# Performance work log

Hardware: AMD Instinct MI355X
Metric: run time of the kernel (lower is better)

Reference implementation:

```python
import jax, jax.numpy as jnp
import numpy as np

B, C, TX, TY = 32, 384, 512, 2048
NL, K = 2, 3
EPS = 1e-5


def _ln(x, g, b):
    # channel-wise LayerNorm over dim 1 of [B, C, T]
    m = jnp.mean(x, axis=1, keepdims=True)
    v = jnp.mean((x - m) ** 2, axis=1, keepdims=True)
    return (x - m) * jax.lax.rsqrt(v + EPS) * g[None, :, None] + b[None, :, None]


def _conv(x, w, b):
    # x: [B, C, T], w: [O, I, K] -> 'SAME' padding == kernel_size // 2 for odd K
    y = jax.lax.conv_general_dilated(x, w, (1,), 'SAME',
                                     dimension_numbers=('NCH', 'OIH', 'NCH'))
    return y + b[None, :, None]


def _variance_predictor(x, mask, lng, lnb, cw, cb, ow, ob):
    # NL x (LayerNorm -> Conv1d -> SiLU -> [dropout=identity in eval]) * mask
    for i in range(NL):
        h = _conv(_ln(x, lng[i], lnb[i]), cw[i], cb[i])
        x = jax.nn.silu(h) * mask
    return _conv(x, ow, ob) * mask  # [B, 1, T]


def setup_inputs() -> dict:
    key = jax.random.key(0)
    it = iter(jax.random.split(key, 16))
    s = 0.02
    d = {}
    d['x'] = jax.random.normal(next(it), (B, C, TX), jnp.float32)
    d['x_mask'] = jnp.ones((B, 1, TX), jnp.float32)
    d['y_mask'] = jnp.ones((B, 1, TY), jnp.float32)
    d['pitch'] = jax.random.normal(next(it), (B, C, TY), jnp.float32)
    d['energy'] = jax.random.normal(next(it), (B, C, TY), jnp.float32)
    d['path'] = jax.random.uniform(next(it), (B, TX, TY), jnp.float32)
    for p in ('dur', 'pit', 'ene'):
        d[p + '_lng'] = jnp.ones((NL, C), jnp.float32)
        d[p + '_lnb'] = jnp.zeros((NL, C), jnp.float32)
        d[p + '_cw'] = jax.random.normal(next(it), (NL, C, C, K), jnp.float32) * s
        d[p + '_cb'] = jnp.zeros((NL, C), jnp.float32)
        d[p + '_ow'] = jax.random.normal(next(it), (1, C, 1), jnp.float32) * s
        d[p + '_ob'] = jnp.zeros((1,), jnp.float32)
    return d


def reference(x, x_mask, y_mask, pitch, energy, path,
              dur_lng, dur_lnb, dur_cw, dur_cb, dur_ow, dur_ob,
              pit_lng, pit_lnb, pit_cw, pit_cb, pit_ow, pit_ob,
              ene_lng, ene_lnb, ene_cw, ene_cb, ene_ow, ene_ob):
    dur_pred = _variance_predictor(x, x_mask, dur_lng, dur_lnb, dur_cw, dur_cb, dur_ow, dur_ob)
    # LengthRegulator: bmm against duration path matrix [B, TX, TY]
    xe = jnp.einsum('bct,bty->bcy', x, path)  # [B, C, TY]
    pitch_pred = _variance_predictor(xe, y_mask, pit_lng, pit_lnb, pit_cw, pit_cb, pit_ow, pit_ob)
    energy_pred = _variance_predictor(xe, y_mask, ene_lng, ene_lnb, ene_cw, ene_cb, ene_ow, ene_ob)
    out = xe + pitch + energy
    return (out, dur_pred, pitch_pred, energy_pred)
```

## Files before the change

### kernel.cpp

```cpp
#include <hip/hip_runtime.h>

#define B_ 32
#define C_ 384
#define TX_ 512
#define TY_ 2048
#define KW_ 3
#define EPS_ 1e-5f
#define LAY_ ((size_t)(36 * 1536 * 8))

typedef __attribute__((ext_vector_type(8))) short short8;
typedef __attribute__((ext_vector_type(4))) float f32x4;

#define MFMA(a, b, c) __builtin_amdgcn_mfma_f32_16x16x32_bf16(a, b, c, 0, 0, 0)

#define WAITV0() do { asm volatile("s_waitcnt vmcnt(0)"); \
                      __builtin_amdgcn_sched_barrier(0); } while (0)
#define WAITL()  do { asm volatile("s_waitcnt lgkmcnt(0)"); \
                      __builtin_amdgcn_sched_barrier(0); } while (0)

typedef unsigned int u32;
__device__ __forceinline__ void gl_lds16(const void* g, void* l) {
    __builtin_amdgcn_global_load_lds(
        (const __attribute__((address_space(1))) u32*)g,
        (__attribute__((address_space(3))) u32*)l, 16, 0, 0);
}

__device__ inline unsigned short f2bf(float f) {
    union { float f; unsigned int u; } v; v.f = f;
    unsigned int r = v.u + 0x7fffu + ((v.u >> 16) & 1u);
    return (unsigned short)(r >> 16);
}
__device__ inline float bf2f(unsigned short s) {
    union { float f; unsigned int u; } v; v.u = ((unsigned int)s) << 16;
    return v.f;
}

template<bool INBF>
__device__ inline float ldx(const void* p, size_t i) {
    if constexpr (INBF) return bf2f(((const unsigned short*)p)[i]);
    else return ((const float*)p)[i];
}

__global__ __launch_bounds__(256) void pack_w2(const float* cw0, const float* cw1,
                                               const float* cw2, const float* g0,
                                               const float* g1, const float* g2,
                                               unsigned short* wp) {
    int idx = blockIdx.x * 256 + threadIdx.x;
    const int NG = 6 * 36 * 384 * 4;
    if (idx >= NG) return;
    int lg = idx & 3;
    int o = (idx >> 2) % 384;
    int c = ((idx >> 2) / 384) % 36;
    int lay = (idx >> 2) / (384 * 36);
    int k = c / 12, ib = c % 12;
    int pr = lay >> 1, l = lay & 1;
    const float* cw = ((pr == 0) ? cw0 : (pr == 1) ? cw1 : cw2) + (size_t)l * C_ * C_ * KW_;
    const float* g  = ((pr == 0) ? g0  : (pr == 1) ? g1  : g2)  + (size_t)l * C_;
    const int i0 = ib * 32 + lg * 8;
    short8 v;
    #pragma unroll
    for (int e = 0; e < 8; e++)
        v[e] = (short)f2bf(cw[((size_t)o * C_ + i0 + e) * KW_ + k] * g[i0 + e]);
    *(short8*)&wp[(size_t)idx * 8] = v;
}

__global__ __launch_bounds__(256) void bias_fold(
    const float* cw0, const float* cw1, const float* cw2,
    const float* be0, const float* be1, const float* be2,
    const float* cb0, const float* cb1, const float* cb2,
    float* biasT, float* bc0, float* bc2) {
    int idx = blockIdx.x * 256 + threadIdx.x;
    if (idx >= 6 * 384) return;
    int o = idx % 384, lay = idx / 384;
    int pr = lay >> 1, l = lay & 1;
    const float* cw = ((pr == 0) ? cw0 : (pr == 1) ? cw1 : cw2)
                      + (size_t)l * C_ * C_ * KW_ + (size_t)o * C_ * KW_;
    const float* be = ((pr == 0) ? be0 : (pr == 1) ? be1 : be2) + (size_t)l * C_;
    const float* cb = ((pr == 0) ? cb0 : (pr == 1) ? cb1 : cb2) + (size_t)l * C_;
    float s0 = 0.f, s1 = 0.f, s2 = 0.f;
    for (int i = 0; i < C_; i++) {
        const float b = be[i];
        s0 += cw[i * 3 + 0] * b; s1 += cw[i * 3 + 1] * b; s2 += cw[i * 3 + 2] * b;
    }
    biasT[idx] = cb[o] + s0 + s1 + s2;
    bc0[idx] = s0; bc2[idx] = s2;
}

__global__ __launch_bounds__(256) void pack_x2(const float* x, unsigned short* xp) {
    int idx = blockIdx.x * 256 + threadIdx.x;
    const int NG = B_ * 16 * 384 * 4;
    if (idx >= NG) return;
    int lg = idx & 3;
    int c = (idx >> 2) % 384;
    int q = ((idx >> 2) / 384) % 16;
    int b = (idx >> 2) / (384 * 16);
    const float* src = x + ((size_t)b * C_ + c) * TX_ + q * 32 + lg * 8;
    short8 v;
    #pragma unroll
    for (int e = 0; e < 8; e++) v[e] = (short)f2bf(src[e]);
    *(short8*)&xp[(size_t)idx * 8] = v;
}

__global__ __launch_bounds__(256) void ln_stats_f32(const float* x, float2* st, int T) {
    __shared__ float r1[4][64], r2[4][64];
    int b = blockIdx.y, t0 = blockIdx.x * 64;
    int tl = threadIdx.x & 63, g = threadIdx.x >> 6;
    int t = t0 + tl;
    const float* p = x + (size_t)b * C_ * T + t;
    float s = 0.f, ss = 0.f;
    for (int c = g; c < C_; c += 4) { float v = p[(size_t)c * T]; s += v; ss += v * v; }
    r1[g][tl] = s; r2[g][tl] = ss;
    __syncthreads();
    if (threadIdx.x < 64) {
        float s1 = r1[0][tl] + r1[1][tl] + r1[2][tl] + r1[3][tl];
        float s2 = r2[0][tl] + r2[1][tl] + r2[2][tl] + r2[3][tl];
        float m = s1 * (1.f / C_);
        float var = s2 * (1.f / C_) - m * m;
        st[(size_t)b * T + t0 + tl] = make_float2(m, rsqrtf(var + EPS_));
    }
}

template<bool INBF>
__global__ __launch_bounds__(512, 4) void fused_vp(
    const void* __restrict__ Xin, const float2* __restrict__ stin,
    const unsigned short* __restrict__ W2lay,
    const float* __restrict__ bT,
    const float* __restrict__ c0v, const float* __restrict__ c2v,
    const float* __restrict__ mask,
    float* __restrict__ pred, const float* __restrict__ ow,
    const float* __restrict__ obias, int T)
{
    __shared__ __align__(16) unsigned short xs[68 * 384];
    __shared__ __align__(16) unsigned short wlds[8][1536];
    float*  red = (float*) &xs[66 * 384];
    float2* st2 = (float2*)&xs[67 * 384];

    const int tid = threadIdx.x;
    const int b = blockIdx.y;
    const int t0 = blockIdx.x * 64;
    const int lane = tid & 63;
    const int wave = tid >> 6;
    const int lr = lane & 15, lg = lane >> 4;
    const int wm = wave * 48;

    const unsigned short* gbw = W2lay + (size_t)((wm + lr) * 4 + lg) * 8;
    const unsigned short* gbw2 = gbw + LAY_;
    auto STAGE = [&](const unsigned short* base, int c) {
        #pragma unroll
        for (int fm = 0; fm < 3; fm++)
            gl_lds16(base + (size_t)c * 12288 + fm * 512, &wlds[wave][fm * 512]);
    };
    STAGE(gbw, 0);

    {
        const int tt = 2 + lane;
        const int t = t0 + lane;
        const float2 mr = stin[(size_t)b * T + t];
        for (int cg = wave; cg < 48; cg += 8) {
            const size_t base = ((size_t)b * C_ + cg * 8) * T + t;
            short8 v8;
            #pragma unroll
            for (int j = 0; j < 8; j++)
                v8[j] = (short)f2bf((ldx<INBF>(Xin, base + (size_t)j * T) - mr.x) * mr.y);
            const int ph = (cg & ~7) | ((cg ^ tt) & 7);
            *(short8*)&xs[tt * 384 + ph * 8] = v8;
        }
        if (tid < 192) {
            const int q = tid / 48;
            const int tt2 = (q < 2) ? q : 64 + q;
            const int cg = tid % 48;
            const int t2 = t0 - 2 + tt2;
            short8 v8;
            if (t2 >= 0 && t2 < T) {
                const float2 mr2 = stin[(size_t)b * T + t2];
                const size_t base = ((size_t)b * C_ + cg * 8) * T + t2;
                #pragma unroll
                for (int j = 0; j < 8; j++)
                    v8[j] = (short)f2bf((ldx<INBF>(Xin, base + (size_t)j * T) - mr2.x) * mr2.y);
            } else {
                #pragma unroll
                for (int j = 0; j < 8; j++) v8[j] = 0;
            }
            const int ph = (cg & ~7) | ((cg ^ tt2) & 7);
            *(short8*)&xs[tt2 * 384 + ph * 8] = v8;
        }
    }
    __syncthreads();

    f32x4 acc[3][5];
    const f32x4 zero = {0.f, 0.f, 0.f, 0.f};
    #pragma unroll
    for (int fm = 0; fm < 3; fm++)
        #pragma unroll
        for (int fn = 0; fn < 5; fn++) acc[fm][fn] = zero;

    for (int c = 0; c < 36; ++c) {
        WAITV0();
        short8 af[3], bf[5];
        #pragma unroll
        for (int fm = 0; fm < 3; fm++)
            af[fm] = *(const short8*)&wlds[wave][fm * 512 + lane * 8];
        const int k = c / 12, ib = c - k * 12;
        const int cgi = ib * 4 + lg;
        #pragma unroll
        for (int fn = 0; fn < 4; fn++) {
            const int row = 1 + fn * 16 + lr + k;
            const int ph = (cgi & ~7) | ((cgi ^ row) & 7);
            bf[fn] = *(const short8*)&xs[row * 384 + ph * 8];
        }
        {
            const int row = (lr == 1) ? (65 + k) : k;
            const int ph = (cgi & ~7) | ((cgi ^ row) & 7);
            bf[4] = *(const short8*)&xs[row * 384 + ph * 8];
        }
        WAITL();
        if (c < 35) STAGE(gbw, c + 1); else STAGE(gbw2, 0);
        __builtin_amdgcn_sched_barrier(0);
        __builtin_amdgcn_s_setprio(1);
        #pragma unroll
        for (int fm = 0; fm < 3; fm++)
            #pragma unroll
            for (int fn = 0; fn < 5; fn++)
                acc[fm][fn] = MFMA(af[fm], bf[fn], acc[fm][fn]);
        __builtin_amdgcn_s_setprio(0);
    }

    __syncthreads();
    if (tid < 132) red[tid] = 0.f;
    __syncthreads();

    #pragma unroll
    for (int fn = 0; fn < 4; fn++) {
        const int tt_h = 1 + fn * 16 + lr;
        const int t = t0 + fn * 16 + lr;
        const float mk = mask[(size_t)b * T + t];
        float s1 = 0.f, s2 = 0.f;
        #pragma unroll
        for (int fm = 0; fm < 3; fm++) {
            const int o0 = wm + fm * 16 + lg * 4;
            #pragma unroll
            for (int j = 0; j < 4; j++) {
                float h = acc[fm][fn][j] + bT[o0 + j];
                if (t == 0) h -= c0v[o0 + j];
                if (t == T - 1) h -= c2v[o0 + j];
                const float y = h * (1.f / (1.f + __expf(-h))) * mk;
                acc[fm][fn][j] = y;
                s1 += y; s2 += y * y;
            }
        }
        atomicAdd(&red[tt_h * 2], s1);
        atomicAdd(&red[tt_h * 2 + 1], s2);
    }
    {
        const int tt_h = (lr == 1) ? 65 : 0;
        const int t = t0 - 1 + tt_h;
        const bool inr = (lr < 2) && (t >= 0) && (t < T);
        const float mk = inr ? mask[(size_t)b * T + t] : 0.f;
        float s1 = 0.f, s2 = 0.f;
        #pragma unroll
        for (int fm = 0; fm < 3; fm++) {
            const int o0 = wm + fm * 16 + lg * 4;
            #pragma unroll
            for (int j = 0; j < 4; j++) {
                const float h = acc[fm][4][j] + bT[o0 + j];
                const float y = inr ? (h * (1.f / (1.f + __expf(-h))) * mk) : 0.f;
                acc[fm][4][j] = y;
                s1 += y; s2 += y * y;
            }
        }
        if (inr) {
            atomicAdd(&red[tt_h * 2], s1);
            atomicAdd(&red[tt_h * 2 + 1], s2);
        }
    }
    __syncthreads();

    if (tid < 66) {
        const float s1 = red[tid * 2], s2 = red[tid * 2 + 1];
        const float m = s1 * (1.f / C_);
        const float var = s2 * (1.f / C_) - m * m;
        st2[tid] = make_float2(m, rsqrtf(var + EPS_));
    }
    __syncthreads();

    #pragma unroll
    for (int fn = 0; fn < 4; fn++) {
        const int tt_h = 1 + fn * 16 + lr;
        const float2 mr = st2[tt_h];
        #pragma unroll
        for (int fm = 0; fm < 3; fm++) {
            ushort4 pk;
            #pragma unroll
            for (int j = 0; j < 4; j++)
                ((unsigned short*)&pk)[j] = f2bf((acc[fm][fn][j] - mr.x) * mr.y);
            const int cg = ((wm + fm * 16) >> 3) + (lg >> 1);
            const int ph = (cg & ~7) | ((cg ^ tt_h) & 7);
            *(ushort4*)&xs[tt_h * 384 + ph * 8 + (lg & 1) * 4] = pk;
        }
    }
    if (lr < 2) {
        const int tt_h = (lr == 1) ? 65 : 0;
        const float2 mr = st2[tt_h];
        #pragma unroll
        for (int fm = 0; fm < 3; fm++) {
            ushort4 pk;
            #pragma unroll
            for (int j = 0; j < 4; j++)
                ((unsigned short*)&pk)[j] = f2bf((acc[fm][4][j] - mr.x) * mr.y);
            const int cg = ((wm + fm * 16) >> 3) + (lg >> 1);
            const int ph = (cg & ~7) | ((cg ^ tt_h) & 7);
            *(ushort4*)&xs[tt_h * 384 + ph * 8 + (lg & 1) * 4] = pk;
        }
    }
    __syncthreads();

    f32x4 acc2[3][4];
    #pragma unroll
    for (int fm = 0; fm < 3; fm++)
        #pragma unroll
        for (int fn = 0; fn < 4; fn++) acc2[fm][fn] = zero;

    for (int c = 0; c < 36; ++c) {
        WAITV0();
        short8 af[3], bf[4];
        #pragma unroll
        for (int fm = 0; fm < 3; fm++)
            af[fm] = *(const short8*)&wlds[wave][fm * 512 + lane * 8];
        const int k = c / 12, ib = c - k * 12;
        const int cgi = ib * 4 + lg;
        #pragma unroll
        for (int fn = 0; fn < 4; fn++) {
            const int row = fn * 16 + lr + k;
            const int ph = (cgi & ~7) | ((cgi ^ row) & 7);
            bf[fn] = *(const short8*)&xs[row * 384 + ph * 8];
        }
        WAITL();
        if (c < 35) STAGE(gbw2, c + 1);
        __builtin_amdgcn_sched_barrier(0);
        __builtin_amdgcn_s_setprio(1);
        #pragma unroll
        for (int fm = 0; fm < 3; fm++)
            #pragma unroll
            for (int fn = 0; fn < 4; fn++)
                acc2[fm][fn] = MFMA(af[fm], bf[fn], acc2[fm][fn]);
        __builtin_amdgcn_s_setprio(0);
    }

    __syncthreads();
    if (tid < 64) red[tid] = 0.f;
    __syncthreads();
    #pragma unroll
    for (int fn = 0; fn < 4; fn++) {
        const int tl = fn * 16 + lr;
        const int t = t0 + tl;
        const float mk = mask[(size_t)b * T + t];
        float s1 = 0.f;
        #pragma unroll
        for (int fm = 0; fm < 3; fm++) {
            const int o0 = wm + fm * 16 + lg * 4;
            #pragma unroll
            for (int j = 0; j < 4; j++) {
                float h = acc2[fm][fn][j] + bT[384 + o0 + j];
                if (t == 0) h -= c0v[384 + o0 + j];
                if (t == T - 1) h -= c2v[384 + o0 + j];
                const float y = h * (1.f / (1.f + __expf(-h))) * mk;
                s1 += y * ow[o0 + j];
            }
        }
        atomicAdd(&red[tl], s1);
    }
    __syncthreads();
    if (tid < 64) {
        const int t = t0 + tid;
        pred[(size_t)b * T + t] = (red[tid] + obias[0]) * mask[(size_t)b * T + t];
    }
}

__global__ __launch_bounds__(512, 4) void bmm_ln(
    const unsigned short* __restrict__ x2, const float* __restrict__ path,
    const float* __restrict__ pitch, const float* __restrict__ energy,
    float* __restrict__ out, unsigned short* __restrict__ xebf,
    float2* __restrict__ stout, int fused)
{
    __shared__ __align__(16) unsigned short ps[32 * 512];
    __shared__ __align__(16) unsigned short wlds[8][1536];
    const int tid = threadIdx.x;
    const int bid = blockIdx.x;
    const int work = (bid & 7) * 256 + (bid >> 3);
    const int b = work >> 6;
    const int y0 = (work & 63) << 5;
    const int lane = tid & 63;
    const int wave = tid >> 6;
    const int lr = lane & 15, lg = lane >> 4;
    const int wm = wave * 48;

    const unsigned short* gbx = x2 + ((size_t)b * 16 * 1536 + (size_t)((wm + lr) * 4 + lg)) * 8;
    auto STAGE = [&](int u) {
        #pragma unroll
        for (int fm = 0; fm < 3; fm++)
            gl_lds16(gbx + (size_t)u * 12288 + fm * 512, &wlds[wave][fm * 512]);
    };
    STAGE(0);

    {
        const int yy = lane & 31;
        const int half = lane >> 5;
        const int gbase = (wave * 2 + half) * 4;
        const float* pb = path + (size_t)b * TX_ * TY_ + y0 + yy;
        float vv[4][8];
        #pragma unroll
        for (int i = 0; i < 4; i++) {
            const int cg = gbase + i;
            #pragma unroll
            for (int j = 0; j < 8; j++) vv[i][j] = pb[(size_t)(cg * 8 + j) * TY_];
        }
        #pragma unroll
        for (int i = 0; i < 4; i++) {
            const int cg = gbase + i;
            short8 v8;
            #pragma unroll
            for (int j = 0; j < 8; j++) v8[j] = (short)f2bf(vv[i][j]);
            const int ph = (cg & ~7) | ((cg ^ yy) & 7);
            *(short8*)&ps[yy * 512 + ph * 8] = v8;
        }
    }
    __syncthreads();

    f32x4 acc[3][2];
    const f32x4 zero = {0.f, 0.f, 0.f, 0.f};
    #pragma unroll
    for (int fm = 0; fm < 3; fm++) { acc[fm][0] = zero; acc[fm][1] = zero; }

    for (int u = 0; u < 16; ++u) {
        WAITV0();
        short8 af[3], bf[2];
        #pragma unroll
        for (int fm = 0; fm < 3; fm++)
            af[fm] = *(const short8*)&wlds[wave][fm * 512 + lane * 8];
        const int cgi = u * 4 + lg;
        #pragma unroll
        for (int fn = 0; fn < 2; fn++) {
            const int row = fn * 16 + lr;
            const int ph = (cgi & ~7) | ((cgi ^ row) & 7);
            bf[fn] = *(const short8*)&ps[row * 512 + ph * 8];
        }
        WAITL();
        if (u < 15) STAGE(u + 1);
        __builtin_amdgcn_sched_barrier(0);
        __builtin_amdgcn_s_setprio(1);
        #pragma unroll
        for (int fm = 0; fm < 3; fm++) {
            acc[fm][0] = MFMA(af[fm], bf[0], acc[fm][0]);
            acc[fm][1] = MFMA(af[fm], bf[1], acc[fm][1]);
        }
        __builtin_amdgcn_s_setprio(0);
    }

    __syncthreads();
    float* red = (float*)ps;
    if (tid < 64) red[tid] = 0.f;
    __syncthreads();

    #pragma unroll
    for (int fn = 0; fn < 2; fn++) {
        const int yl = fn * 16 + lr;
        const int y = y0 + yl;
        float s1 = 0.f, s2 = 0.f;
        #pragma unroll
        for (int fm = 0; fm < 3; fm++) {
            #pragma unroll
            for (int j = 0; j < 4; j++) {
                const int c = wm + fm * 16 + lg * 4 + j;
                const size_t gi = ((size_t)b * C_ + c) * TY_ + y;
                const float v = acc[fm][fn][j];
                if (fused) {
                    out[gi] = v + pitch[gi] + energy[gi];
                    xebf[gi] = f2bf(v);
                } else {
                    out[gi] = v;
                }
                s1 += v; s2 += v * v;
            }
        }
        atomicAdd(&red[yl * 2], s1);
        atomicAdd(&red[yl * 2 + 1], s2);
    }
    __syncthreads();
    if (tid < 32) {
        const int y = y0 + tid;
        const float s1 = red[tid * 2], s2 = red[tid * 2 + 1];
        const float m = s1 * (1.f / C_);
        const float var = s2 * (1.f / C_) - m * m;
        stout[(size_t)b * TY_ + y] = make_float2(m, rsqrtf(var + EPS_));
    }
}

__global__ __launch_bounds__(256) void add3(float4* o, const float4* p, const float4* e, int n4) {
    for (int i = blockIdx.x * 256 + threadIdx.x; i < n4; i += gridDim.x * 256) {
        float4 a = o[i], x1 = p[i], x2 = e[i];
        a.x += x1.x + x2.x; a.y += x1.y + x2.y;
        a.z += x1.z + x2.z; a.w += x1.w + x2.w;
        o[i] = a;
    }
}

extern "C" void kernel_launch(void* const* d_in, const int* in_sizes, int n_in,
                              void* d_out, int out_size, void* d_ws, size_t ws_size,
                              hipStream_t stream)
{
    const float* x      = (const float*)d_in[0];
    const float* x_mask = (const float*)d_in[1];
    const float* y_mask = (const float*)d_in[2];
    const float* pitch  = (const float*)d_in[3];
    const float* energy = (const float*)d_in[4];
    const float* path   = (const float*)d_in[5];
    const float* prm[3][6];
    for (int p = 0; p < 3; p++)
        for (int q = 0; q < 6; q++)
            prm[p][q] = (const float*)d_in[6 + p * 6 + q];

    float* out         = (float*)d_out;
    float* dur_pred    = out + (size_t)B_ * C_ * TY_;
    float* pitch_pred  = dur_pred + B_ * TX_;
    float* energy_pred = pitch_pred + B_ * TY_;

    const size_t BCTY = (size_t)B_ * C_ * TY_;
    char* w = (char*)d_ws;
    auto alloc = [&](size_t bytes) { char* r = w; w += (bytes + 255) & ~(size_t)255; return r; };

    unsigned short* W2   = (unsigned short*)alloc(6 * LAY_ * 2);
    float* biasT         = (float*)alloc(6 * 384 * 4);
    float* bc0           = (float*)alloc(6 * 384 * 4);
    float* bc2           = (float*)alloc(6 * 384 * 4);
    float2* stA          = (float2*)alloc((size_t)B_ * TY_ * 8);
    unsigned short* x2p  = (unsigned short*)alloc((size_t)B_ * 196608 * 2);
    size_t base_end = (size_t)(w - (char*)d_ws);
    unsigned short* xebf = (unsigned short*)alloc(BCTY * 2);
    size_t xe_end = (size_t)(w - (char*)d_ws);

    const bool haveXe = (xe_end <= ws_size);
    if (base_end > ws_size) return;

    pack_w2<<<dim3((6 * 36 * 384 * 4 + 255) / 256), 256, 0, stream>>>(
        prm[0][2], prm[1][2], prm[2][2], prm[0][0], prm[1][0], prm[2][0], W2);
    bias_fold<<<dim3(9), 256, 0, stream>>>(
        prm[0][2], prm[1][2], prm[2][2], prm[0][1], prm[1][1], prm[2][1],
        prm[0][3], prm[1][3], prm[2][3], biasT, bc0, bc2);
    pack_x2<<<dim3((B_ * 16 * 384 * 4 + 255) / 256), 256, 0, stream>>>(x, x2p);
    ln_stats_f32<<<dim3(TX_ / 64, B_), 256, 0, stream>>>(x, stA, TX_);

    fused_vp<false><<<dim3(TX_ / 64, B_), 512, 0, stream>>>(
        x, stA, W2, biasT, bc0, bc2, x_mask,
        dur_pred, prm[0][4], prm[0][5], TX_);

    bmm_ln<<<dim3(2048, 1, 1), 512, 0, stream>>>(
        x2p, path, pitch, energy, out, haveXe ? xebf : nullptr, stA, haveXe ? 1 : 0);

    if (haveXe) {
        fused_vp<true><<<dim3(TY_ / 64, B_), 512, 0, stream>>>(
            xebf, stA, W2 + 2 * LAY_, biasT + 2 * 384, bc0 + 2 * 384, bc2 + 2 * 384,
            y_mask, pitch_pred, prm[1][4], prm[1][5], TY_);
        fused_vp<true><<<dim3(TY_ / 64, B_), 512, 0, stream>>>(
            xebf, stA, W2 + 4 * LAY_, biasT + 4 * 384, bc0 + 4 * 384, bc2 + 4 * 384,
            y_mask, energy_pred, prm[2][4], prm[2][5], TY_);
    } else {
        fused_vp<false><<<dim3(TY_ / 64, B_), 512, 0, stream>>>(
            out, stA, W2 + 2 * LAY_, biasT + 2 * 384, bc0 + 2 * 384, bc2 + 2 * 384,
            y_mask, pitch_pred, prm[1][4], prm[1][5], TY_);
        fused_vp<false><<<dim3(TY_ / 64, B_), 512, 0, stream>>>(
            out, stA, W2 + 4 * LAY_, biasT + 4 * 384, bc0 + 4 * 384, bc2 + 4 * 384,
            y_mask, energy_pred, prm[2][4], prm[2][5], TY_);
        add3<<<dim3(2048), 256, 0, stream>>>((float4*)out, (const float4*)pitch,
                                             (const float4*)energy, B_ * C_ * TY_ / 4);
    }
}
```

Measured before the change: 644.3 us.

## Double the fused predictor time tile and double-buffer weight staging

The fused variance-predictor kernel now covers 128 time steps per block instead of 64. Each staged weight tile therefore feeds twice as many MFMAs, and the per-block weight traffic is amortised over more work. Weight staging in both fused_vp and bmm_ln moves from a single LDS buffer to two buffers with a two-ahead prefetch and partial vmcnt waits, so global loads overlap compute. The cost is much more LDS and more accumulator registers, so launch bounds drop to 2 blocks per CU and the grids have half as many blocks, which lowers occupancy.

```diff
diff --git a/kernel.cpp b/kernel.cpp
--- a/kernel.cpp
+++ b/kernel.cpp
@@ -4,7 +4,6 @@
 #define C_ 384
 #define TX_ 512
 #define TY_ 2048
-#define KW_ 3
 #define EPS_ 1e-5f
 #define LAY_ ((size_t)(36 * 1536 * 8))
 
@@ -13,7 +12,7 @@
 
 #define MFMA(a, b, c) __builtin_amdgcn_mfma_f32_16x16x32_bf16(a, b, c, 0, 0, 0)
 
-#define WAITV0() do { asm volatile("s_waitcnt vmcnt(0)"); \
+#define WAITV(N) do { asm volatile("s_waitcnt vmcnt(" #N ")"); \
                       __builtin_amdgcn_sched_barrier(0); } while (0)
 #define WAITL()  do { asm volatile("s_waitcnt lgkmcnt(0)"); \
                       __builtin_amdgcn_sched_barrier(0); } while (0)
@@ -54,13 +53,13 @@
     int lay = (idx >> 2) / (384 * 36);
     int k = c / 12, ib = c % 12;
     int pr = lay >> 1, l = lay & 1;
-    const float* cw = ((pr == 0) ? cw0 : (pr == 1) ? cw1 : cw2) + (size_t)l * C_ * C_ * KW_;
+    const float* cw = ((pr == 0) ? cw0 : (pr == 1) ? cw1 : cw2) + (size_t)l * C_ * C_ * 3;
     const float* g  = ((pr == 0) ? g0  : (pr == 1) ? g1  : g2)  + (size_t)l * C_;
     const int i0 = ib * 32 + lg * 8;
     short8 v;
     #pragma unroll
     for (int e = 0; e < 8; e++)
-        v[e] = (short)f2bf(cw[((size_t)o * C_ + i0 + e) * KW_ + k] * g[i0 + e]);
+        v[e] = (short)f2bf(cw[((size_t)o * C_ + i0 + e) * 3 + k] * g[i0 + e]);
     *(short8*)&wp[(size_t)idx * 8] = v;
 }
 
@@ -74,7 +73,7 @@
     int o = idx % 384, lay = idx / 384;
     int pr = lay >> 1, l = lay & 1;
     const float* cw = ((pr == 0) ? cw0 : (pr == 1) ? cw1 : cw2)
-                      + (size_t)l * C_ * C_ * KW_ + (size_t)o * C_ * KW_;
+                      + (size_t)l * C_ * C_ * 3 + (size_t)o * C_ * 3;
     const float* be = ((pr == 0) ? be0 : (pr == 1) ? be1 : be2) + (size_t)l * C_;
     const float* cb = ((pr == 0) ? cb0 : (pr == 1) ? cb1 : cb2) + (size_t)l * C_;
     float s0 = 0.f, s1 = 0.f, s2 = 0.f;
@@ -121,7 +120,7 @@
 }
 
 template<bool INBF>
-__global__ __launch_bounds__(512, 4) void fused_vp(
+__global__ __launch_bounds__(512, 2) void fused_vp(
     const void* __restrict__ Xin, const float2* __restrict__ stin,
     const unsigned short* __restrict__ W2lay,
     const float* __restrict__ bT,
@@ -130,14 +129,14 @@
     float* __restrict__ pred, const float* __restrict__ ow,
     const float* __restrict__ obias, int T)
 {
-    __shared__ __align__(16) unsigned short xs[68 * 384];
-    __shared__ __align__(16) unsigned short wlds[8][1536];
-    float*  red = (float*) &xs[66 * 384];
-    float2* st2 = (float2*)&xs[67 * 384];
+    __shared__ __align__(16) unsigned short xs[132 * 384];
+    __shared__ __align__(16) unsigned short wlds[8][2][1536];
+    __shared__ float red[260];
+    __shared__ float2 st2[130];
 
     const int tid = threadIdx.x;
     const int b = blockIdx.y;
-    const int t0 = blockIdx.x * 64;
+    const int t0 = blockIdx.x * 128;
     const int lane = tid & 63;
     const int wave = tid >> 6;
     const int lr = lane & 15, lg = lane >> 4;
@@ -145,18 +144,22 @@
 
     const unsigned short* gbw = W2lay + (size_t)((wm + lr) * 4 + lg) * 8;
     const unsigned short* gbw2 = gbw + LAY_;
-    auto STAGE = [&](const unsigned short* base, int c) {
-        #pragma unroll
-        for (int fm = 0; fm < 3; fm++)
-            gl_lds16(base + (size_t)c * 12288 + fm * 512, &wlds[wave][fm * 512]);
+    auto STAGE = [&](const unsigned short* base, int c, int buf) {
+        #pragma unroll
+        for (int fm = 0; fm < 3; fm++)
+            gl_lds16(base + (size_t)c * 12288 + fm * 512, &wlds[wave][buf][fm * 512]);
     };
-    STAGE(gbw, 0);
+    STAGE(gbw, 0, 0);
+    STAGE(gbw, 1, 1);
 
     {
-        const int tt = 2 + lane;
-        const int t = t0 + lane;
+        const int tl = tid & 127;
+        const int tt = 2 + tl;
+        const int t = t0 + tl;
         const float2 mr = stin[(size_t)b * T + t];
-        for (int cg = wave; cg < 48; cg += 8) {
+        const int cg0 = (tid >> 7) * 12;
+        for (int i = 0; i < 12; i++) {
+            const int cg = cg0 + i;
             const size_t base = ((size_t)b * C_ + cg * 8) * T + t;
             short8 v8;
             #pragma unroll
@@ -167,7 +170,7 @@
         }
         if (tid < 192) {
             const int q = tid / 48;
-            const int tt2 = (q < 2) ? q : 64 + q;
+            const int tt2 = (q < 2) ? q : 128 + q;
             const int cg = tid % 48;
             const int t2 = t0 - 2 + tt2;
             short8 v8;
@@ -187,50 +190,51 @@
     }
     __syncthreads();
 
-    f32x4 acc[3][5];
+    f32x4 acc[3][9];
     const f32x4 zero = {0.f, 0.f, 0.f, 0.f};
     #pragma unroll
     for (int fm = 0; fm < 3; fm++)
         #pragma unroll
-        for (int fn = 0; fn < 5; fn++) acc[fm][fn] = zero;
+        for (int fn = 0; fn < 9; fn++) acc[fm][fn] = zero;
 
     for (int c = 0; c < 36; ++c) {
-        WAITV0();
-        short8 af[3], bf[5];
-        #pragma unroll
-        for (int fm = 0; fm < 3; fm++)
-            af[fm] = *(const short8*)&wlds[wave][fm * 512 + lane * 8];
+        WAITV(3);
+        short8 af[3], bf[9];
+        #pragma unroll
+        for (int fm = 0; fm < 3; fm++)
+            af[fm] = *(const short8*)&wlds[wave][c & 1][fm * 512 + lane * 8];
         const int k = c / 12, ib = c - k * 12;
         const int cgi = ib * 4 + lg;
         #pragma unroll
-        for (int fn = 0; fn < 4; fn++) {
+        for (int fn = 0; fn < 8; fn++) {
             const int row = 1 + fn * 16 + lr + k;
             const int ph = (cgi & ~7) | ((cgi ^ row) & 7);
             bf[fn] = *(const short8*)&xs[row * 384 + ph * 8];
         }
         {
-            const int row = (lr == 1) ? (65 + k) : k;
+            const int row = (lr == 1) ? (129 + k) : k;
             const int ph = (cgi & ~7) | ((cgi ^ row) & 7);
-            bf[4] = *(const short8*)&xs[row * 384 + ph * 8];
+            bf[8] = *(const short8*)&xs[row * 384 + ph * 8];
         }
         WAITL();
-        if (c < 35) STAGE(gbw, c + 1); else STAGE(gbw2, 0);
+        if (c < 34) STAGE(gbw, c + 2, c & 1);
+        else        STAGE(gbw2, c - 34, c & 1);
         __builtin_amdgcn_sched_barrier(0);
         __builtin_amdgcn_s_setprio(1);
         #pragma unroll
         for (int fm = 0; fm < 3; fm++)
             #pragma unroll
-            for (int fn = 0; fn < 5; fn++)
+            for (int fn = 0; fn < 9; fn++)
                 acc[fm][fn] = MFMA(af[fm], bf[fn], acc[fm][fn]);
         __builtin_amdgcn_s_setprio(0);
     }
 
     __syncthreads();
-    if (tid < 132) red[tid] = 0.f;
-    __syncthreads();
-
-    #pragma unroll
-    for (int fn = 0; fn < 4; fn++) {
+    if (tid < 260) red[tid] = 0.f;
+    __syncthreads();
+
+    #pragma unroll
+    for (int fn = 0; fn < 8; fn++) {
         const int tt_h = 1 + fn * 16 + lr;
         const int t = t0 + fn * 16 + lr;
         const float mk = mask[(size_t)b * T + t];
@@ -252,7 +256,7 @@
         atomicAdd(&red[tt_h * 2 + 1], s2);
     }
     {
-        const int tt_h = (lr == 1) ? 65 : 0;
+        const int tt_h = (lr == 1) ? 129 : 0;
         const int t = t0 - 1 + tt_h;
         const bool inr = (lr < 2) && (t >= 0) && (t < T);
         const float mk = inr ? mask[(size_t)b * T + t] : 0.f;
@@ -262,9 +266,9 @@
             const int o0 = wm + fm * 16 + lg * 4;
             #pragma unroll
             for (int j = 0; j < 4; j++) {
-                const float h = acc[fm][4][j] + bT[o0 + j];
+                const float h = acc[fm][8][j] + bT[o0 + j];
                 const float y = inr ? (h * (1.f / (1.f + __expf(-h))) * mk) : 0.f;
-                acc[fm][4][j] = y;
+                acc[fm][8][j] = y;
                 s1 += y; s2 += y * y;
             }
         }
@@ -275,7 +279,7 @@
     }
     __syncthreads();
 
-    if (tid < 66) {
+    if (tid < 130) {
         const float s1 = red[tid * 2], s2 = red[tid * 2 + 1];
         const float m = s1 * (1.f / C_);
         const float var = s2 * (1.f / C_) - m * m;
@@ -284,7 +288,7 @@
     __syncthreads();
 
     #pragma unroll
-    for (int fn = 0; fn < 4; fn++) {
+    for (int fn = 0; fn < 8; fn++) {
         const int tt_h = 1 + fn * 16 + lr;
         const float2 mr = st2[tt_h];
         #pragma unroll
@@ -299,14 +303,14 @@
         }
     }
     if (lr < 2) {
-        const int tt_h = (lr == 1) ? 65 : 0;
+        const int tt_h = (lr == 1) ? 129 : 0;
         const float2 mr = st2[tt_h];
         #pragma unroll
         for (int fm = 0; fm < 3; fm++) {
             ushort4 pk;
             #pragma unroll
             for (int j = 0; j < 4; j++)
-                ((unsigned short*)&pk)[j] = f2bf((acc[fm][4][j] - mr.x) * mr.y);
+                ((unsigned short*)&pk)[j] = f2bf((acc[fm][8][j] - mr.x) * mr.y);
             const int cg = ((wm + fm * 16) >> 3) + (lg >> 1);
             const int ph = (cg & ~7) | ((cg ^ tt_h) & 7);
             *(ushort4*)&xs[tt_h * 384 + ph * 8 + (lg & 1) * 4] = pk;
@@ -314,43 +318,43 @@
     }
     __syncthreads();
 
-    f32x4 acc2[3][4];
+    f32x4 acc2[3][8];
     #pragma unroll
     for (int fm = 0; fm < 3; fm++)
         #pragma unroll
-        for (int fn = 0; fn < 4; fn++) acc2[fm][fn] = zero;
+        for (int fn = 0; fn < 8; fn++) acc2[fm][fn] = zero;
 
     for (int c = 0; c < 36; ++c) {
-        WAITV0();
-        short8 af[3], bf[4];
-        #pragma unroll
-        for (int fm = 0; fm < 3; fm++)
-            af[fm] = *(const short8*)&wlds[wave][fm * 512 + lane * 8];
+        WAITV(3);
+        short8 af[3], bf[8];
+        #pragma unroll
+        for (int fm = 0; fm < 3; fm++)
+            af[fm] = *(const short8*)&wlds[wave][c & 1][fm * 512 + lane * 8];
         const int k = c / 12, ib = c - k * 12;
         const int cgi = ib * 4 + lg;
         #pragma unroll
-        for (int fn = 0; fn < 4; fn++) {
+        for (int fn = 0; fn < 8; fn++) {
             const int row = fn * 16 + lr + k;
             const int ph = (cgi & ~7) | ((cgi ^ row) & 7);
             bf[fn] = *(const short8*)&xs[row * 384 + ph * 8];
         }
         WAITL();
-        if (c < 35) STAGE(gbw2, c + 1);
+        STAGE(gbw2, (c + 2 < 36) ? c + 2 : 35, c & 1);
         __builtin_amdgcn_sched_barrier(0);
         __builtin_amdgcn_s_setprio(1);
         #pragma unroll
         for (int fm = 0; fm < 3; fm++)
             #pragma unroll
-            for (int fn = 0; fn < 4; fn++)
+            for (int fn = 0; fn < 8; fn++)
                 acc2[fm][fn] = MFMA(af[fm], bf[fn], acc2[fm][fn]);
         __builtin_amdgcn_s_setprio(0);
     }
 
     __syncthreads();
-    if (tid < 64) red[tid] = 0.f;
-    __syncthreads();
-    #pragma unroll
-    for (int fn = 0; fn < 4; fn++) {
+    if (tid < 128) red[tid] = 0.f;
+    __syncthreads();
+    #pragma unroll
+    for (int fn = 0; fn < 8; fn++) {
         const int tl = fn * 16 + lr;
         const int t = t0 + tl;
         const float mk = mask[(size_t)b * T + t];
@@ -370,7 +374,7 @@
         atomicAdd(&red[tl], s1);
     }
     __syncthreads();
-    if (tid < 64) {
+    if (tid < 128) {
         const int t = t0 + tid;
         pred[(size_t)b * T + t] = (red[tid] + obias[0]) * mask[(size_t)b * T + t];
     }
@@ -383,7 +387,7 @@
     float2* __restrict__ stout, int fused)
 {
     __shared__ __align__(16) unsigned short ps[32 * 512];
-    __shared__ __align__(16) unsigned short wlds[8][1536];
+    __shared__ __align__(16) unsigned short wlds[8][2][1536];
     const int tid = threadIdx.x;
     const int bid = blockIdx.x;
     const int work = (bid & 7) * 256 + (bid >> 3);
@@ -395,12 +399,13 @@
     const int wm = wave * 48;
 
     const unsigned short* gbx = x2 + ((size_t)b * 16 * 1536 + (size_t)((wm + lr) * 4 + lg)) * 8;
-    auto STAGE = [&](int u) {
-        #pragma unroll
-        for (int fm = 0; fm < 3; fm++)
-            gl_lds16(gbx + (size_t)u * 12288 + fm * 512, &wlds[wave][fm * 512]);
+    auto STAGE = [&](int u, int buf) {
+        #pragma unroll
+        for (int fm = 0; fm < 3; fm++)
+            gl_lds16(gbx + (size_t)u * 12288 + fm * 512, &wlds[wave][buf][fm * 512]);
     };
-    STAGE(0);
+    STAGE(0, 0);
+    STAGE(1, 1);
 
     {
         const int yy = lane & 31;
@@ -432,11 +437,11 @@
     for (int fm = 0; fm < 3; fm++) { acc[fm][0] = zero; acc[fm][1] = zero; }
 
     for (int u = 0; u < 16; ++u) {
-        WAITV0();
+        WAITV(3);
         short8 af[3], bf[2];
         #pragma unroll
         for (int fm = 0; fm < 3; fm++)
-            af[fm] = *(const short8*)&wlds[wave][fm * 512 + lane * 8];
+            af[fm] = *(const short8*)&wlds[wave][u & 1][fm * 512 + lane * 8];
         const int cgi = u * 4 + lg;
         #pragma unroll
         for (int fn = 0; fn < 2; fn++) {
@@ -445,7 +450,7 @@
             bf[fn] = *(const short8*)&ps[row * 512 + ph * 8];
         }
         WAITL();
-        if (u < 15) STAGE(u + 1);
+        STAGE((u + 2 < 16) ? u + 2 : 15, u & 1);
         __builtin_amdgcn_sched_barrier(0);
         __builtin_amdgcn_s_setprio(1);
         #pragma unroll
@@ -455,6 +460,7 @@
         }
         __builtin_amdgcn_s_setprio(0);
     }
+    WAITV(0);
 
     __syncthreads();
     float* red = (float*)ps;
@@ -549,7 +555,7 @@
     pack_x2<<<dim3((B_ * 16 * 384 * 4 + 255) / 256), 256, 0, stream>>>(x, x2p);
     ln_stats_f32<<<dim3(TX_ / 64, B_), 256, 0, stream>>>(x, stA, TX_);
 
-    fused_vp<false><<<dim3(TX_ / 64, B_), 512, 0, stream>>>(
+    fused_vp<false><<<dim3(TX_ / 128, B_), 512, 0, stream>>>(
         x, stA, W2, biasT, bc0, bc2, x_mask,
         dur_pred, prm[0][4], prm[0][5], TX_);
 
@@ -557,17 +563,17 @@
         x2p, path, pitch, energy, out, haveXe ? xebf : nullptr, stA, haveXe ? 1 : 0);
 
     if (haveXe) {
-        fused_vp<true><<<dim3(TY_ / 64, B_), 512, 0, stream>>>(
+        fused_vp<true><<<dim3(TY_ / 128, B_), 512, 0, stream>>>(
             xebf, stA, W2 + 2 * LAY_, biasT + 2 * 384, bc0 + 2 * 384, bc2 + 2 * 384,
             y_mask, pitch_pred, prm[1][4], prm[1][5], TY_);
-        fused_vp<true><<<dim3(TY_ / 64, B_), 512, 0, stream>>>(
+        fused_vp<true><<<dim3(TY_ / 128, B_), 512, 0, stream>>>(
             xebf, stA, W2 + 4 * LAY_, biasT + 4 * 384, bc0 + 4 * 384, bc2 + 4 * 384,
             y_mask, energy_pred, prm[2][4], prm[2][5], TY_);
     } else {
-        fused_vp<false><<<dim3(TY_ / 64, B_), 512, 0, stream>>>(
+        fused_vp<false><<<dim3(TY_ / 128, B_), 512, 0, stream>>>(
             out, stA, W2 + 2 * LAY_, biasT + 2 * 384, bc0 + 2 * 384, bc2 + 2 * 384,
             y_mask, pitch_pred, prm[1][4], prm[1][5], TY_);
-        fused_vp<false><<<dim3(TY_ / 64, B_), 512, 0, stream>>>(
+        fused_vp<false><<<dim3(TY_ / 128, B_), 512, 0, stream>>>(
             out, stA, W2 + 4 * LAY_, biasT + 4 * 384, bc0 + 4 * 384, bc2 + 4 * 384,
             y_mask, energy_pred, prm[2][4], prm[2][5], TY_);
         add3<<<dim3(2048), 256, 0, stream>>>((float4*)out, (const float4*)pitch,
```

New measurement: 643.9 us. Within noise of the previous version (-0.1%).
